# Kernel optimization log

Measured on AMD Instinct MI355X. Metric: run time of the kernel, lower is better.

The kernel has to match this reference:

```python
import jax, jax.numpy as jnp
import numpy as np

D = 11          # tree depth (root level); leaves at depth 0
B = 16          # trees per batch
D_MODEL = 256   # params.emb_dim
VOCAB = 512     # len(id2word)


def _build_forest():
    """B perfect binary trees, nodes laid out level-by-level (leaves first)."""
    widths = [2 ** (D - k) for k in range(D + 1)]          # nodes per level
    off = np.concatenate([[0], np.cumsum(widths)]).astype(np.int64)
    per = int(off[-1])                                      # 2^(D+1)-1 = 4095
    depths_t = np.concatenate([np.full(w, k, np.int64) for k, w in enumerate(widths)])
    left_t = np.zeros(per, np.int64)
    right_t = np.zeros(per, np.int64)
    for k in range(1, D + 1):
        loc = np.arange(widths[k])
        idx = off[k] + loc
        left_t[idx] = off[k - 1] + 2 * loc
        right_t[idx] = off[k - 1] + 2 * loc + 1
    toff = (np.arange(B) * per)[:, None]                    # global node offsets per tree
    depths = np.tile(depths_t, B)
    left = (left_t[None, :] + toff).reshape(-1)
    right = (right_t[None, :] + toff).reshape(-1)
    leaf_ids = (np.arange(widths[0])[None, :] + toff).reshape(-1)
    internal = np.concatenate([
        (off[k] + np.arange(widths[k])[None, :] + toff).reshape(-1)
        for k in range(1, D + 1)
    ])                                                      # sorted by depth ascending
    return depths, left, right, leaf_ids, internal, per


def setup_inputs() -> dict:
    key = jax.random.key(0)
    k1, k2, k3 = jax.random.split(key, 3)
    depths, left, right, leaf_ids, internal, per = _build_forest()
    N = B * per
    tokens = jax.random.randint(k1, (N,), 0, VOCAB, dtype=jnp.int32)
    # learned params: leaf embedding table (max_norm=1.0 semantics), TreeLSTM cell
    emb = jax.random.normal(k2, (VOCAB, D_MODEL), dtype=jnp.float32) * 0.02
    W = jax.random.normal(k3, (2 * D_MODEL, 5 * D_MODEL), dtype=jnp.float32) / np.sqrt(2.0 * D_MODEL)
    b = jnp.zeros((5 * D_MODEL,), jnp.float32)
    operation_order = jnp.concatenate([jnp.array([-1], jnp.int32), jnp.full((D,), 7, jnp.int32)])
    lengths = jnp.full((B,), per, dtype=jnp.int32)
    return {
        "tokens": tokens,
        "left_idx": jnp.asarray(left, jnp.int32),
        "right_idx": jnp.asarray(right, jnp.int32),
        "depths": jnp.asarray(depths, jnp.int32),
        "operation_order": operation_order,
        "lengths": lengths,
        "leaf_ids": jnp.asarray(leaf_ids, jnp.int32),
        "internal_ids": jnp.asarray(internal, jnp.int32),
        "emb": emb,
        "W": W,
        "b": b,
    }


def _leaf_embed(emb, toks):
    # torch Embedding(max_norm=1.0): rows renormalized to L2 norm <= 1 at lookup
    e = emb[toks]
    nrm = jnp.linalg.norm(e, axis=-1, keepdims=True)
    return e * jnp.minimum(1.0, 1.0 / jnp.maximum(nrm, 1e-7))


def reference(tokens, left_idx, right_idx, depths, operation_order, lengths,
              leaf_ids, internal_ids, emb, W, b):
    N = tokens.shape[0]
    d = emb.shape[1]
    num_steps = operation_order.shape[0]   # = D + 1
    depth = num_steps - 1
    batch = lengths.shape[0]

    # step 0: leaves (operation_order[0] == -1) -> masked_scatter of embeddings
    acts = jnp.zeros((N, d), dtype=emb.dtype).at[leaf_ids].add(_leaf_embed(emb, tokens[leaf_ids]))
    mem = jnp.zeros((N, d), dtype=emb.dtype)   # memory_size = 1, cell state per node

    start = 0
    for k in range(1, depth + 1):
        width = batch * (2 ** (depth - k))      # static per-depth node count
        ids = internal_ids[start:start + width]
        start += width
        li = left_idx[ids]
        ri = right_idx[ids]
        hl, hr = acts[li], acts[ri]             # gather child activations [w, d]
        cl, cr = mem[li], mem[ri]               # gather child cell states [w, d]
        # binary N-ary TreeLSTM cell (_apply_function)
        g = jnp.concatenate([hl, hr], axis=-1) @ W + b   # [w, 5d]
        i, fl, fr, o, u = jnp.split(g, 5, axis=-1)
        c = jax.nn.sigmoid(i) * jnp.tanh(u) + jax.nn.sigmoid(fl) * cl + jax.nn.sigmoid(fr) * cr
        h = jax.nn.sigmoid(o) * jnp.tanh(c)
        # torch_scatter.scatter(...) added onto running buffers
        acts = acts.at[ids].add(h)
        mem = mem.at[ids].add(c)

    # _compute_output: split by equal lengths + pad_sequence -> [B, per_tree, d]
    return acts.reshape(batch, -1, d)
```

## Files before the change

### kernel.cpp

```cpp
#include <hip/hip_runtime.h>
#include <stdint.h>

using bf16   = __bf16;
using bf16x4 = __attribute__((ext_vector_type(4))) __bf16;
using bf16x8 = __attribute__((ext_vector_type(8))) __bf16;
using f32x4  = __attribute__((ext_vector_type(4))) float;

#define DEPTH   11
#define NTREES  16
#define DM      256
#define PER     4095
#define KDIM    512
#define NGATES  5

__device__ __forceinline__ float sigf(float x) { return 1.0f / (1.0f + __expf(-x)); }
__device__ __forceinline__ float tanh_fast(float x) {
    float e = __expf(2.0f * x);
    return 1.0f - 2.0f / (e + 1.0f);
}

__device__ __forceinline__ void load_lds16(const bf16* g, bf16* l) {
    __builtin_amdgcn_global_load_lds((const __attribute__((address_space(1))) void*)g,
                                     (__attribute__((address_space(3))) void*)l,
                                     16, 0, 0);
}

__global__ __launch_bounds__(256) void prep_wfrag(const float* __restrict__ W,
                                                  bf16* __restrict__ Wf) {
    int tid = blockIdx.x * 256 + threadIdx.x;
    int f   = tid >> 6;
    int l   = tid & 63;
    int gt  = f >> 4;
    int ks  = f & 15;
    int n   = (gt << 4) + (l & 15);
    int k0  = (ks << 5) + ((l >> 4) << 3);
    bf16x8 v;
    #pragma unroll
    for (int e = 0; e < 8; ++e) v[e] = (bf16)W[(size_t)(k0 + e) * 1280 + n];
    *reinterpret_cast<bf16x8*>(Wf + (size_t)tid * 8) = v;
}

__global__ __launch_bounds__(256) void leaf_kernel(const int* __restrict__ tokens,
                                                   const float* __restrict__ emb,
                                                   float* acts, bf16* actsb) {
    int wid  = (blockIdx.x * 256 + threadIdx.x) >> 6;
    int lane = threadIdx.x & 63;
    int b    = wid >> 11;
    int loc  = wid & 2047;
    int id   = b * PER + loc;
    int tok  = tokens[id];

    float4 e = *reinterpret_cast<const float4*>(emb + tok * DM + lane * 4);
    float ss = e.x * e.x + e.y * e.y + e.z * e.z + e.w * e.w;
    #pragma unroll
    for (int off = 32; off; off >>= 1) ss += __shfl_xor(ss, off);
    float scale = fminf(1.0f, 1.0f / fmaxf(sqrtf(ss), 1e-7f));
    e.x *= scale; e.y *= scale; e.z *= scale; e.w *= scale;

    int o = id * DM + lane * 4;
    *reinterpret_cast<float4*>(acts + o) = e;
    bf16x4 eb;
    eb.x = (bf16)e.x; eb.y = (bf16)e.y; eb.z = (bf16)e.z; eb.w = (bf16)e.w;
    *reinterpret_cast<bf16x4*>(actsb + o) = eb;
}

template<int RPB>
__global__ __launch_bounds__(256, 2) void level_big(
        const bf16* __restrict__ actsb_in, const bf16* __restrict__ Wfrag,
        const float* __restrict__ bias, float* __restrict__ mem,
        float* __restrict__ acts, bf16* __restrict__ actsb_out,
        int off_k, int off_km1, int zmem) {
    constexpr int NRG = RPB / 16;
    constexpr int NLD = RPB / 32;
    __shared__ __align__(16) bf16 ldsA[2][8][RPB][8];

    int t    = threadIdx.x;
    int lane = t & 63;
    int w    = t >> 6;
    int lo   = lane & 15;
    int hi   = lane >> 4;

    int rt    = blockIdx.x >> 2;
    int uct   = blockIdx.x & 3;
    int b     = blockIdx.y;
    int rm    = rt * RPB;
    int wslot = (uct << 2) + w;

    const bf16* Abase = actsb_in + (size_t)(b * PER + off_km1) * DM;

    const bf16* aSrc[NLD];
    #pragma unroll
    for (int i = 0; i < NLD; ++i) {
        int s   = i * 256 + t;
        aSrc[i] = Abase + (size_t)(rm + (s & (RPB - 1))) * KDIM + (s / RPB) * 8;
    }

    const bf16* bbase = Wfrag + ((size_t)wslot << 13) + lane * 8;

    int ucol = (wslot << 4) + lo;
    float bi[NGATES];
    #pragma unroll
    for (int g = 0; g < NGATES; ++g) bi[g] = bias[g * DM + ucol];

    #pragma unroll
    for (int i = 0; i < NLD; ++i)
        load_lds16(aSrc[i], &ldsA[0][0][0][0] + (i * 256 + t) * 8);

    f32x4 acc[NGATES][NRG] = {};

    __syncthreads();

    for (int kt = 0; kt < 8; ++kt) {
        int cur = kt & 1;
        if (kt < 7) {
            int ko = (kt + 1) * 64;
            #pragma unroll
            for (int i = 0; i < NLD; ++i)
                load_lds16(aSrc[i] + ko, &ldsA[cur ^ 1][0][0][0] + (i * 256 + t) * 8);
        }

        #pragma unroll
        for (int q = 0; q < 2; ++q) {
            bf16x8 bb[NGATES];
            #pragma unroll
            for (int g = 0; g < NGATES; ++g)
                bb[g] = *reinterpret_cast<const bf16x8*>(bbase + (size_t)(((g << 8) + (kt << 1) + q) << 9));
            #pragma unroll
            for (int rg = 0; rg < NRG; ++rg) {
                bf16x8 af = *reinterpret_cast<const bf16x8*>(&ldsA[cur][(q << 2) + hi][(rg << 4) + lo][0]);
                #pragma unroll
                for (int g = 0; g < NGATES; ++g)
                    acc[g][rg] = __builtin_amdgcn_mfma_f32_16x16x32_bf16(af, bb[g], acc[g][rg], 0, 0, 0);
            }
        }
        __syncthreads();
    }

    int treebase = b * PER;
    #pragma unroll
    for (int rg = 0; rg < NRG; ++rg) {
        #pragma unroll
        for (int r = 0; r < 4; ++r) {
            int ml = rm + (rg << 4) + (hi << 2) + r;
            int id = treebase + off_k + ml;
            float cl = 0.0f, cr = 0.0f;
            if (!zmem) {
                int ch = (treebase + off_km1 + (ml << 1)) * DM + ucol;
                cl = mem[ch];
                cr = mem[ch + DM];
            }
            float gi = acc[0][rg][r] + bi[0];
            float gl = acc[1][rg][r] + bi[1];
            float gr = acc[2][rg][r] + bi[2];
            float go = acc[3][rg][r] + bi[3];
            float gu = acc[4][rg][r] + bi[4];
            float c  = sigf(gi) * tanh_fast(gu) + sigf(gl) * cl + sigf(gr) * cr;
            float h  = sigf(go) * tanh_fast(c);
            int oi = id * DM + ucol;
            acts[oi]      = h;
            mem[oi]       = c;
            actsb_out[oi] = (bf16)h;
        }
    }
}

__global__ __launch_bounds__(256) void level_kernel(
        const bf16* __restrict__ actsb_in, const bf16* __restrict__ Wfrag,
        const float* __restrict__ bias, float* mem, float* acts, bf16* actsb_out,
        int off_k, int off_km1, int shift) {
    int wid  = blockIdx.x * 4 + (threadIdx.x >> 6);
    int lane = threadIdx.x & 63;
    int tile = wid >> 4;
    int uc   = wid & 15;
    int m0   = tile << 4;
    int lo   = lane & 15;
    int hi   = lane >> 4;
    int mask = (1 << shift) - 1;

    int mA   = m0 + lo;
    int rowA = (mA >> shift) * PER + off_km1 + ((mA & mask) << 1);
    const bf16* aptr = actsb_in + (size_t)rowA * DM + hi * 8;

    const bf16* bbase = Wfrag + ((size_t)uc << 13) + lane * 8;

    int ucol = (uc << 4) + lo;
    float bi[NGATES];
    #pragma unroll
    for (int g = 0; g < NGATES; ++g) bi[g] = bias[g * DM + ucol];

    f32x4 acc[NGATES] = {};

    #pragma unroll
    for (int kt = 0; kt < KDIM / 32; ++kt) {
        bf16x8 a = *reinterpret_cast<const bf16x8*>(aptr + kt * 32);
        #pragma unroll
        for (int g = 0; g < NGATES; ++g) {
            bf16x8 bb = *reinterpret_cast<const bf16x8*>(bbase + (size_t)(((g << 8) + kt) << 9));
            acc[g] = __builtin_amdgcn_mfma_f32_16x16x32_bf16(a, bb, acc[g], 0, 0, 0);
        }
    }

    #pragma unroll
    for (int r = 0; r < 4; ++r) {
        int m   = m0 + (hi << 2) + r;
        int tb  = (m >> shift) * PER;
        int loc = m & mask;
        int id  = tb + off_k + loc;
        int ch  = (tb + off_km1 + (loc << 1)) * DM + ucol;
        float cl = mem[ch];
        float cr = mem[ch + DM];
        float gi = acc[0][r] + bi[0];
        float gl = acc[1][r] + bi[1];
        float gr = acc[2][r] + bi[2];
        float go = acc[3][r] + bi[3];
        float gu = acc[4][r] + bi[4];
        float c  = sigf(gi) * tanh_fast(gu) + sigf(gl) * cl + sigf(gr) * cr;
        float h  = sigf(go) * tanh_fast(c);
        int oi = id * DM + ucol;
        acts[oi]      = h;
        mem[oi]       = c;
        actsb_out[oi] = (bf16)h;
    }
}

extern "C" void kernel_launch(void* const* d_in, const int* in_sizes, int n_in,
                              void* d_out, int out_size, void* d_ws, size_t ws_size,
                              hipStream_t stream) {
    (void)in_sizes; (void)n_in; (void)out_size; (void)ws_size;
    const int*   tokens = (const int*)d_in[0];
    const float* emb    = (const float*)d_in[8];
    const float* W      = (const float*)d_in[9];
    const float* bias   = (const float*)d_in[10];
    float* acts = (float*)d_out;

    char* ws = (char*)d_ws;
    bf16*  Wfrag = (bf16*)ws;
    bf16*  actsb = (bf16*)(ws + 1310720);
    float* mem   = (float*)(ws + 1310720 + 33546240);

    prep_wfrag<<<dim3(320), dim3(256), 0, stream>>>(W, Wfrag);
    leaf_kernel<<<dim3(8192), dim3(256), 0, stream>>>(tokens, emb, acts, actsb);

    int off_km1 = 0;
    for (int k = 1; k <= DEPTH; ++k) {
        int shift   = DEPTH - k;
        int Mt      = 1 << shift;
        int off_k   = off_km1 + (Mt << 1);
        int M_total = NTREES << shift;
        if (Mt >= 512) {
            level_big<128><<<dim3((Mt / 128) * 4, NTREES), dim3(256), 0, stream>>>(
                actsb, Wfrag, bias, mem, acts, actsb, off_k, off_km1, (k == 1) ? 1 : 0);
        } else if (Mt >= 128) {
            level_big<64><<<dim3((Mt / 64) * 4, NTREES), dim3(256), 0, stream>>>(
                actsb, Wfrag, bias, mem, acts, actsb, off_k, off_km1, 0);
        } else {
            level_kernel<<<dim3(M_total / 4), dim3(256), 0, stream>>>(
                actsb, Wfrag, bias, mem, acts, actsb, off_k, off_km1, shift);
        }
        off_km1 = off_k;
    }
}
```

Baseline: 191.7 us.

## Prefetch W fragments into register double buffer and use fine-grained vmcnt barriers

The big-level GEMM kernel is fixed to 64 rows per block and used for every level with at least 128 nodes per tree, dropping the 128-row variant. Weight fragments for the next k-tile are now loaded into a double-buffered register array alongside the LDS prefetch. __syncthreads is replaced by an explicit s_waitcnt vmcnt(10) plus s_barrier, so the next tile's loads can stay in flight during the wait, and the k loop is fully unrolled with sched_barriers to keep the order fixed. This costs more registers and relies on a hand-counted vmcnt being correct, and the big levels now run with smaller tiles and twice as many blocks.

```diff
diff --git a/kernel.cpp b/kernel.cpp
--- a/kernel.cpp
+++ b/kernel.cpp
@@ -64,12 +64,12 @@
     *reinterpret_cast<bf16x4*>(actsb + o) = eb;
 }
 
-template<int RPB>
 __global__ __launch_bounds__(256, 2) void level_big(
         const bf16* __restrict__ actsb_in, const bf16* __restrict__ Wfrag,
         const float* __restrict__ bias, float* __restrict__ mem,
         float* __restrict__ acts, bf16* __restrict__ actsb_out,
         int off_k, int off_km1, int zmem) {
+    constexpr int RPB = 64;
     constexpr int NRG = RPB / 16;
     constexpr int NLD = RPB / 32;
     __shared__ __align__(16) bf16 ldsA[2][8][RPB][8];
@@ -105,11 +105,22 @@
     #pragma unroll
     for (int i = 0; i < NLD; ++i)
         load_lds16(aSrc[i], &ldsA[0][0][0][0] + (i * 256 + t) * 8);
+    bf16x8 bb[2][NGATES][2];
+    #pragma unroll
+    for (int g = 0; g < NGATES; ++g)
+        #pragma unroll
+        for (int q = 0; q < 2; ++q)
+            bb[0][g][q] = *reinterpret_cast<const bf16x8*>(bbase + (size_t)(((g << 8) | q) << 9));
 
     f32x4 acc[NGATES][NRG] = {};
 
-    __syncthreads();
-
+    __builtin_amdgcn_sched_barrier(0);
+    asm volatile("s_waitcnt vmcnt(10)" ::: "memory");
+    __builtin_amdgcn_sched_barrier(0);
+    __builtin_amdgcn_s_barrier();
+    __builtin_amdgcn_sched_barrier(0);
+
+    #pragma unroll
     for (int kt = 0; kt < 8; ++kt) {
         int cur = kt & 1;
         if (kt < 7) {
@@ -117,23 +128,33 @@
             #pragma unroll
             for (int i = 0; i < NLD; ++i)
                 load_lds16(aSrc[i] + ko, &ldsA[cur ^ 1][0][0][0] + (i * 256 + t) * 8);
-        }
-
-        #pragma unroll
-        for (int q = 0; q < 2; ++q) {
-            bf16x8 bb[NGATES];
             #pragma unroll
             for (int g = 0; g < NGATES; ++g)
-                bb[g] = *reinterpret_cast<const bf16x8*>(bbase + (size_t)(((g << 8) + (kt << 1) + q) << 9));
+                #pragma unroll
+                for (int q = 0; q < 2; ++q)
+                    bb[cur ^ 1][g][q] = *reinterpret_cast<const bf16x8*>(
+                        bbase + (size_t)(((g << 8) | ((kt + 1) * 2 + q)) << 9));
+        }
+        __builtin_amdgcn_sched_barrier(0);
+
+        #pragma unroll
+        for (int q = 0; q < 2; ++q) {
             #pragma unroll
             for (int rg = 0; rg < NRG; ++rg) {
                 bf16x8 af = *reinterpret_cast<const bf16x8*>(&ldsA[cur][(q << 2) + hi][(rg << 4) + lo][0]);
                 #pragma unroll
                 for (int g = 0; g < NGATES; ++g)
-                    acc[g][rg] = __builtin_amdgcn_mfma_f32_16x16x32_bf16(af, bb[g], acc[g][rg], 0, 0, 0);
+                    acc[g][rg] = __builtin_amdgcn_mfma_f32_16x16x32_bf16(af, bb[cur][g][q], acc[g][rg], 0, 0, 0);
             }
         }
-        __syncthreads();
+        __builtin_amdgcn_sched_barrier(0);
+
+        if (kt < 7) {
+            asm volatile("s_waitcnt vmcnt(10)" ::: "memory");
+            __builtin_amdgcn_sched_barrier(0);
+            __builtin_amdgcn_s_barrier();
+            __builtin_amdgcn_sched_barrier(0);
+        }
     }
 
     int treebase = b * PER;
@@ -247,12 +268,9 @@
         int Mt      = 1 << shift;
         int off_k   = off_km1 + (Mt << 1);
         int M_total = NTREES << shift;
-        if (Mt >= 512) {
-            level_big<128><<<dim3((Mt / 128) * 4, NTREES), dim3(256), 0, stream>>>(
+        if (Mt >= 128) {
+            level_big<<<dim3((Mt / 64) * 4, NTREES), dim3(256), 0, stream>>>(
                 actsb, Wfrag, bias, mem, acts, actsb, off_k, off_km1, (k == 1) ? 1 : 0);
-        } else if (Mt >= 128) {
-            level_big<64><<<dim3((Mt / 64) * 4, NTREES), dim3(256), 0, stream>>>(
-                actsb, Wfrag, bias, mem, acts, actsb, off_k, off_km1, 0);
         } else {
             level_kernel<<<dim3(M_total / 4), dim3(256), 0, stream>>>(
                 actsb, Wfrag, bias, mem, acts, actsb, off_k, off_km1, shift);
```

Result: faster. 184.5 us (-3.7%).

## Replace LDS-staged double-buffered A tiles with direct global fragment loads

Applied to the files above, without the earlier changes.

The big-level kernel no longer stages child activations through shared memory with async global-to-LDS copies and double buffering. Each lane now loads its MFMA A fragments straight from global memory, and the k-loop is fully unrolled with no barriers. All large levels also switch to a single 64-row tile instead of 128 rows for the widest levels. This removes LDS traffic and __syncthreads, but reads are less coalesced, there is more redundant global traffic across the four column-tile blocks, and the widest levels launch more blocks.

```diff
diff --git a/kernel.cpp b/kernel.cpp
--- a/kernel.cpp
+++ b/kernel.cpp
@@ -17,12 +17,6 @@
 __device__ __forceinline__ float tanh_fast(float x) {
     float e = __expf(2.0f * x);
     return 1.0f - 2.0f / (e + 1.0f);
-}
-
-__device__ __forceinline__ void load_lds16(const bf16* g, bf16* l) {
-    __builtin_amdgcn_global_load_lds((const __attribute__((address_space(1))) void*)g,
-                                     (__attribute__((address_space(3))) void*)l,
-                                     16, 0, 0);
 }
 
 __global__ __launch_bounds__(256) void prep_wfrag(const float* __restrict__ W,
@@ -64,16 +58,11 @@
     *reinterpret_cast<bf16x4*>(actsb + o) = eb;
 }
 
-template<int RPB>
 __global__ __launch_bounds__(256, 2) void level_big(
         const bf16* __restrict__ actsb_in, const bf16* __restrict__ Wfrag,
         const float* __restrict__ bias, float* __restrict__ mem,
         float* __restrict__ acts, bf16* __restrict__ actsb_out,
         int off_k, int off_km1, int zmem) {
-    constexpr int NRG = RPB / 16;
-    constexpr int NLD = RPB / 32;
-    __shared__ __align__(16) bf16 ldsA[2][8][RPB][8];
-
     int t    = threadIdx.x;
     int lane = t & 63;
     int w    = t >> 6;
@@ -83,17 +72,15 @@
     int rt    = blockIdx.x >> 2;
     int uct   = blockIdx.x & 3;
     int b     = blockIdx.y;
-    int rm    = rt * RPB;
+    int rm    = rt << 6;
     int wslot = (uct << 2) + w;
 
     const bf16* Abase = actsb_in + (size_t)(b * PER + off_km1) * DM;
 
-    const bf16* aSrc[NLD];
-    #pragma unroll
-    for (int i = 0; i < NLD; ++i) {
-        int s   = i * 256 + t;
-        aSrc[i] = Abase + (size_t)(rm + (s & (RPB - 1))) * KDIM + (s / RPB) * 8;
-    }
+    const bf16* aptr[4];
+    #pragma unroll
+    for (int rg = 0; rg < 4; ++rg)
+        aptr[rg] = Abase + (size_t)(rm + (rg << 4) + lo) * KDIM + hi * 8;
 
     const bf16* bbase = Wfrag + ((size_t)wslot << 13) + lane * 8;
 
@@ -102,43 +89,28 @@
     #pragma unroll
     for (int g = 0; g < NGATES; ++g) bi[g] = bias[g * DM + ucol];
 
-    #pragma unroll
-    for (int i = 0; i < NLD; ++i)
-        load_lds16(aSrc[i], &ldsA[0][0][0][0] + (i * 256 + t) * 8);
-
-    f32x4 acc[NGATES][NRG] = {};
-
-    __syncthreads();
-
-    for (int kt = 0; kt < 8; ++kt) {
-        int cur = kt & 1;
-        if (kt < 7) {
-            int ko = (kt + 1) * 64;
+    f32x4 acc[NGATES][4] = {};
+
+    #pragma unroll
+    for (int ks = 0; ks < 16; ++ks) {
+        bf16x8 a[4];
+        #pragma unroll
+        for (int rg = 0; rg < 4; ++rg)
+            a[rg] = *reinterpret_cast<const bf16x8*>(aptr[rg] + ks * 32);
+        bf16x8 bb[NGATES];
+        #pragma unroll
+        for (int g = 0; g < NGATES; ++g)
+            bb[g] = *reinterpret_cast<const bf16x8*>(bbase + (size_t)(((g << 8) | ks) << 9));
+        #pragma unroll
+        for (int g = 0; g < NGATES; ++g)
             #pragma unroll
-            for (int i = 0; i < NLD; ++i)
-                load_lds16(aSrc[i] + ko, &ldsA[cur ^ 1][0][0][0] + (i * 256 + t) * 8);
-        }
-
-        #pragma unroll
-        for (int q = 0; q < 2; ++q) {
-            bf16x8 bb[NGATES];
-            #pragma unroll
-            for (int g = 0; g < NGATES; ++g)
-                bb[g] = *reinterpret_cast<const bf16x8*>(bbase + (size_t)(((g << 8) + (kt << 1) + q) << 9));
-            #pragma unroll
-            for (int rg = 0; rg < NRG; ++rg) {
-                bf16x8 af = *reinterpret_cast<const bf16x8*>(&ldsA[cur][(q << 2) + hi][(rg << 4) + lo][0]);
-                #pragma unroll
-                for (int g = 0; g < NGATES; ++g)
-                    acc[g][rg] = __builtin_amdgcn_mfma_f32_16x16x32_bf16(af, bb[g], acc[g][rg], 0, 0, 0);
-            }
-        }
-        __syncthreads();
+            for (int rg = 0; rg < 4; ++rg)
+                acc[g][rg] = __builtin_amdgcn_mfma_f32_16x16x32_bf16(a[rg], bb[g], acc[g][rg], 0, 0, 0);
     }
 
     int treebase = b * PER;
     #pragma unroll
-    for (int rg = 0; rg < NRG; ++rg) {
+    for (int rg = 0; rg < 4; ++rg) {
         #pragma unroll
         for (int r = 0; r < 4; ++r) {
             int ml = rm + (rg << 4) + (hi << 2) + r;
@@ -247,12 +219,9 @@
         int Mt      = 1 << shift;
         int off_k   = off_km1 + (Mt << 1);
         int M_total = NTREES << shift;
-        if (Mt >= 512) {
-            level_big<128><<<dim3((Mt / 128) * 4, NTREES), dim3(256), 0, stream>>>(
+        if (Mt >= 128) {
+            level_big<<<dim3((Mt / 64) * 4, NTREES), dim3(256), 0, stream>>>(
                 actsb, Wfrag, bias, mem, acts, actsb, off_k, off_km1, (k == 1) ? 1 : 0);
-        } else if (Mt >= 128) {
-            level_big<64><<<dim3((Mt / 64) * 4, NTREES), dim3(256), 0, stream>>>(
-                actsb, Wfrag, bias, mem, acts, actsb, off_k, off_km1, 0);
         } else {
             level_kernel<<<dim3(M_total / 4), dim3(256), 0, stream>>>(
                 actsb, Wfrag, bias, mem, acts, actsb, off_k, off_km1, shift);
```

New measurement: 201.3 us. +5.0%, slower.

## Use split-K reduction for small tree levels and unify big levels at 64 rows

Applied to the files above, without the earlier changes.

For small levels (fewer than 128 nodes per tree), each block now computes one 16-row by 16-column tile with its four waves splitting the K dimension. Partial sums are reduced through shared memory, which gives four times as many waves for latency hiding on the serial deep levels. The large-level kernel always uses 64-row tiles with a higher occupancy hint (4 blocks per CU), replacing the 128-row variant for the widest levels. This trades extra LDS reduction and a barrier, plus less reuse of W per block on the big levels, for more parallelism.

```diff
diff --git a/kernel.cpp b/kernel.cpp
--- a/kernel.cpp
+++ b/kernel.cpp
@@ -64,14 +64,14 @@
     *reinterpret_cast<bf16x4*>(actsb + o) = eb;
 }
 
-template<int RPB>
-__global__ __launch_bounds__(256, 2) void level_big(
+__global__ __launch_bounds__(256, 4) void level_big(
         const bf16* __restrict__ actsb_in, const bf16* __restrict__ Wfrag,
         const float* __restrict__ bias, float* __restrict__ mem,
         float* __restrict__ acts, bf16* __restrict__ actsb_out,
         int off_k, int off_km1, int zmem) {
-    constexpr int NRG = RPB / 16;
-    constexpr int NLD = RPB / 32;
+    constexpr int RPB = 64;
+    constexpr int NRG = 4;
+    constexpr int NLD = 2;
     __shared__ __align__(16) bf16 ldsA[2][8][RPB][8];
 
     int t    = threadIdx.x;
@@ -124,7 +124,7 @@
             bf16x8 bb[NGATES];
             #pragma unroll
             for (int g = 0; g < NGATES; ++g)
-                bb[g] = *reinterpret_cast<const bf16x8*>(bbase + (size_t)(((g << 8) + (kt << 1) + q) << 9));
+                bb[g] = *reinterpret_cast<const bf16x8*>(bbase + (size_t)(((g << 8) | ((kt << 1) + q)) << 9));
             #pragma unroll
             for (int rg = 0; rg < NRG; ++rg) {
                 bf16x8 af = *reinterpret_cast<const bf16x8*>(&ldsA[cur][(q << 2) + hi][(rg << 4) + lo][0]);
@@ -164,35 +164,32 @@
     }
 }
 
-__global__ __launch_bounds__(256) void level_kernel(
+__global__ __launch_bounds__(256) void level_splitk(
         const bf16* __restrict__ actsb_in, const bf16* __restrict__ Wfrag,
         const float* __restrict__ bias, float* mem, float* acts, bf16* actsb_out,
         int off_k, int off_km1, int shift) {
-    int wid  = blockIdx.x * 4 + (threadIdx.x >> 6);
-    int lane = threadIdx.x & 63;
-    int tile = wid >> 4;
-    int uc   = wid & 15;
-    int m0   = tile << 4;
+    __shared__ f32x4 red[3][NGATES][64];
+
+    int t    = threadIdx.x;
+    int lane = t & 63;
+    int w    = t >> 6;
     int lo   = lane & 15;
     int hi   = lane >> 4;
+    int tile = blockIdx.x >> 4;
+    int uc   = blockIdx.x & 15;
+    int m0   = tile << 4;
     int mask = (1 << shift) - 1;
 
     int mA   = m0 + lo;
     int rowA = (mA >> shift) * PER + off_km1 + ((mA & mask) << 1);
-    const bf16* aptr = actsb_in + (size_t)rowA * DM + hi * 8;
-
+    const bf16* aptr  = actsb_in + (size_t)rowA * DM + hi * 8 + (w << 2) * 32;
     const bf16* bbase = Wfrag + ((size_t)uc << 13) + lane * 8;
 
-    int ucol = (uc << 4) + lo;
-    float bi[NGATES];
-    #pragma unroll
-    for (int g = 0; g < NGATES; ++g) bi[g] = bias[g * DM + ucol];
-
     f32x4 acc[NGATES] = {};
-
-    #pragma unroll
-    for (int kt = 0; kt < KDIM / 32; ++kt) {
-        bf16x8 a = *reinterpret_cast<const bf16x8*>(aptr + kt * 32);
+    #pragma unroll
+    for (int kk = 0; kk < 4; ++kk) {
+        int kt = (w << 2) + kk;
+        bf16x8 a = *reinterpret_cast<const bf16x8*>(aptr + kk * 32);
         #pragma unroll
         for (int g = 0; g < NGATES; ++g) {
             bf16x8 bb = *reinterpret_cast<const bf16x8*>(bbase + (size_t)(((g << 8) + kt) << 9));
@@ -200,26 +197,41 @@
         }
     }
 
-    #pragma unroll
-    for (int r = 0; r < 4; ++r) {
-        int m   = m0 + (hi << 2) + r;
-        int tb  = (m >> shift) * PER;
-        int loc = m & mask;
-        int id  = tb + off_k + loc;
-        int ch  = (tb + off_km1 + (loc << 1)) * DM + ucol;
-        float cl = mem[ch];
-        float cr = mem[ch + DM];
-        float gi = acc[0][r] + bi[0];
-        float gl = acc[1][r] + bi[1];
-        float gr = acc[2][r] + bi[2];
-        float go = acc[3][r] + bi[3];
-        float gu = acc[4][r] + bi[4];
-        float c  = sigf(gi) * tanh_fast(gu) + sigf(gl) * cl + sigf(gr) * cr;
-        float h  = sigf(go) * tanh_fast(c);
-        int oi = id * DM + ucol;
-        acts[oi]      = h;
-        mem[oi]       = c;
-        actsb_out[oi] = (bf16)h;
+    if (w) {
+        #pragma unroll
+        for (int g = 0; g < NGATES; ++g) red[w - 1][g][lane] = acc[g];
+    }
+    __syncthreads();
+    if (w == 0) {
+        int ucol = (uc << 4) + lo;
+        float bi[NGATES];
+        #pragma unroll
+        for (int g = 0; g < NGATES; ++g) {
+            f32x4 p0 = red[0][g][lane], p1 = red[1][g][lane], p2 = red[2][g][lane];
+            acc[g] += p0 + p1 + p2;
+            bi[g] = bias[g * DM + ucol];
+        }
+        #pragma unroll
+        for (int r = 0; r < 4; ++r) {
+            int m   = m0 + (hi << 2) + r;
+            int tb  = (m >> shift) * PER;
+            int loc = m & mask;
+            int id  = tb + off_k + loc;
+            int ch  = (tb + off_km1 + (loc << 1)) * DM + ucol;
+            float cl = mem[ch];
+            float cr = mem[ch + DM];
+            float gi = acc[0][r] + bi[0];
+            float gl = acc[1][r] + bi[1];
+            float gr = acc[2][r] + bi[2];
+            float go = acc[3][r] + bi[3];
+            float gu = acc[4][r] + bi[4];
+            float c  = sigf(gi) * tanh_fast(gu) + sigf(gl) * cl + sigf(gr) * cr;
+            float h  = sigf(go) * tanh_fast(c);
+            int oi = id * DM + ucol;
+            acts[oi]      = h;
+            mem[oi]       = c;
+            actsb_out[oi] = (bf16)h;
+        }
     }
 }
 
@@ -247,14 +259,11 @@
         int Mt      = 1 << shift;
         int off_k   = off_km1 + (Mt << 1);
         int M_total = NTREES << shift;
-        if (Mt >= 512) {
-            level_big<128><<<dim3((Mt / 128) * 4, NTREES), dim3(256), 0, stream>>>(
+        if (Mt >= 128) {
+            level_big<<<dim3((Mt / 64) * 4, NTREES), dim3(256), 0, stream>>>(
                 actsb, Wfrag, bias, mem, acts, actsb, off_k, off_km1, (k == 1) ? 1 : 0);
-        } else if (Mt >= 128) {
-            level_big<64><<<dim3((Mt / 64) * 4, NTREES), dim3(256), 0, stream>>>(
-                actsb, Wfrag, bias, mem, acts, actsb, off_k, off_km1, 0);
         } else {
-            level_kernel<<<dim3(M_total / 4), dim3(256), 0, stream>>>(
+            level_splitk<<<dim3(M_total), dim3(256), 0, stream>>>(
                 actsb, Wfrag, bias, mem, acts, actsb, off_k, off_km1, shift);
         }
         off_km1 = off_k;
```

Measured after the change: 190.4 us. No clear change (-0.7%).
